# Performance work log

Measured on AMD Instinct MI355X. Metric: run time of the kernel, lower is better.

Reference implementation:

```python
import jax, jax.numpy as jnp
import numpy as np

B, L, T = 8192, 1024, 4  # batch, seq_len, n_tags (BMES)


def setup_inputs() -> dict:
    key = jax.random.key(0)
    k1, k2, k3, k4, k5 = jax.random.split(key, 5)
    return {
        "s_tag": jax.random.normal(k1, (B, L, T), dtype=jnp.float32),
        "tags": jax.random.randint(k2, (B, L), 0, T),
        "mask": jnp.ones((B, L), dtype=bool),
        "trans_score": (jax.random.normal(k3, (T, T), dtype=jnp.float32) * 0.1),
        "start_score": (jax.random.normal(k4, (T,), dtype=jnp.float32) * 0.1),
        "end_score": (jax.random.normal(k5, (T,), dtype=jnp.float32) * 0.1),
    }


def reference(s_tag, tags, mask, trans_score, start_score, end_score):
    # forward() path of LinearCRFWordSegmentation: loss = (logZ - gold_score)/B.
    # Note: forward calls set_mask(False), so the structural masks are unused.
    b, l, t = s_tag.shape
    bidx = jnp.arange(b)
    end_pos = mask.sum(axis=-1) - 1  # [B] index of last valid position

    # ---- gold path score (get_scores) ----
    emit = jnp.take_along_axis(s_tag, tags[..., None], axis=-1)[..., 0]  # [B,L]
    trans = trans_score[tags[:, :-1], tags[:, 1:]]                        # [B,L-1]
    per_pos = emit + jnp.pad(trans, ((0, 0), (1, 0)))                     # [B,L]
    score = jnp.sum(jnp.where(mask, per_pos, jnp.float32(0)))
    score = score + start_score[tags[:, 0]].sum()
    score = score + end_score[tags[bidx, end_pos]].sum()

    # ---- log partition (crf): sequential logsumexp recurrence over tags ----
    s0 = s_tag[:, 0] + start_score  # [B,T]

    def step(s_prev, emit_t):
        # [B,T_prev,1] + [1,T_prev,T_cur] + [B,1,T_cur] -> logsumexp over prev
        s_new = jax.nn.logsumexp(
            s_prev[:, :, None] + trans_score[None] + emit_t[:, None, :], axis=1
        )
        return s_new, s_new

    emits = jnp.swapaxes(s_tag, 0, 1)  # [L,B,T]
    _, ss = jax.lax.scan(step, s0, emits[1:])      # [L-1,B,T]
    ss = jnp.concatenate([s0[None], ss], axis=0)    # [L,B,T] alpha trellis
    final = ss[end_pos, bidx] + end_score           # [B,T]
    logZ = jax.nn.logsumexp(final, axis=-1).sum()

    return (logZ - score) / jnp.float32(b)
```

## Files before the change

### kernel.cpp

```cpp
#include <hip/hip_runtime.h>

#define Bn 8192
#define Ln 1024

#define LOG2E 1.4426950408889634f
#define LN2f  0.6931471805599453f

typedef float f32x2 __attribute__((ext_vector_type(2)));
typedef __attribute__((address_space(3))) void lds_void_t;
typedef const __attribute__((address_space(1))) void gbl_void_t;

__device__ __forceinline__ float sel4(float4 v, int t) {
    float r = v.x;
    r = (t == 1) ? v.y : r;
    r = (t == 2) ? v.z : r;
    r = (t == 3) ? v.w : r;
    return r;
}

__device__ __forceinline__ float rfl(float x) {
    return __int_as_float(__builtin_amdgcn_readfirstlane(__float_as_int(x)));
}

__device__ __forceinline__ f32x2 pkmax(f32x2 a, f32x2 b) {
    return (f32x2){fmaxf(a.x, b.x), fmaxf(a.y, b.y)};
}

__global__ __launch_bounds__(64) void crf_half(
    const float* __restrict__ s_tag, const int* __restrict__ tags,
    const float* __restrict__ trans,
    float* __restrict__ wsP, int* __restrict__ wsK, float* __restrict__ wsS)
{
    __shared__ float4 sS[512];

    const int lw = threadIdx.x;
    const int b  = blockIdx.x >> 1;
    const int h  = blockIdx.x & 1;

    const float4* __restrict__ srow = (const float4*)s_tag + (size_t)b * Ln + h * 512;
    const int*    __restrict__ trow = tags + (size_t)b * Ln + h * 512;

#pragma unroll
    for (int k = 0; k < 8; k++) {
        int s = k * 64 + lw;
        int g = s ^ ((s >> 3) & 7);
        __builtin_amdgcn_global_load_lds((gbl_void_t*)(srow + g),
                                         (lds_void_t*)(&sS[k * 64]), 16, 0, 0);
    }

    const int4* trow4 = (const int4*)(trow + 8 * lw);
    int4 ta = trow4[0], tb = trow4[1];
    int tg[8] = {ta.x, ta.y, ta.z, ta.w, tb.x, tb.y, tb.z, tb.w};
    int prevtag = 0;
    if (!(h == 0 && lw == 0)) prevtag = trow[8 * lw - 1];

    float trsum = 0.f;
    {
        int pt = prevtag;
#pragma unroll
        for (int j = 0; j < 8; j++) {
            if (!(h == 0 && lw == 0 && j == 0)) trsum += trans[pt * 4 + tg[j]];
            pt = tg[j];
        }
    }
    float es[4][4];
#pragma unroll
    for (int k = 0; k < 4; k++)
#pragma unroll
        for (int j = 0; j < 4; j++)
            es[k][j] = rfl(exp2f(trans[k * 4 + j] * LOG2E));

    asm volatile("s_waitcnt vmcnt(0)" ::: "memory");

    float4 st[8];
#pragma unroll
    for (int j = 0; j < 8; j++)
        st[j] = sS[8 * lw + (j ^ (lw & 7))];

    f32x2 pc[4][2];
#pragma unroll
    for (int j = 0; j < 4; j++) {
        pc[j][0] = (f32x2){(j == 0) ? 1.f : 0.f, (j == 1) ? 1.f : 0.f};
        pc[j][1] = (f32x2){(j == 2) ? 1.f : 0.f, (j == 3) ? 1.f : 0.f};
    }
    int scale = 0;
    float emitsum = 0.f;

#pragma unroll
    for (int j = 0; j < 8; j++) {
        emitsum += sel4(st[j], tg[j]);
        if (!(j == 0 && lw == 0 && h == 0)) {
            float f0 = exp2f(st[j].x * LOG2E);
            float f1 = exp2f(st[j].y * LOG2E);
            float f2 = exp2f(st[j].z * LOG2E);
            float f3 = exp2f(st[j].w * LOG2E);

            f32x2 n00 = pc[0][0] * es[0][0] + pc[1][0] * es[1][0] + pc[2][0] * es[2][0] + pc[3][0] * es[3][0];
            f32x2 n01 = pc[0][1] * es[0][0] + pc[1][1] * es[1][0] + pc[2][1] * es[2][0] + pc[3][1] * es[3][0];
            f32x2 n10 = pc[0][0] * es[0][1] + pc[1][0] * es[1][1] + pc[2][0] * es[2][1] + pc[3][0] * es[3][1];
            f32x2 n11 = pc[0][1] * es[0][1] + pc[1][1] * es[1][1] + pc[2][1] * es[2][1] + pc[3][1] * es[3][1];
            f32x2 n20 = pc[0][0] * es[0][2] + pc[1][0] * es[1][2] + pc[2][0] * es[2][2] + pc[3][0] * es[3][2];
            f32x2 n21 = pc[0][1] * es[0][2] + pc[1][1] * es[1][2] + pc[2][1] * es[2][2] + pc[3][1] * es[3][2];
            f32x2 n30 = pc[0][0] * es[0][3] + pc[1][0] * es[1][3] + pc[2][0] * es[2][3] + pc[3][0] * es[3][3];
            f32x2 n31 = pc[0][1] * es[0][3] + pc[1][1] * es[1][3] + pc[2][1] * es[2][3] + pc[3][1] * es[3][3];
            pc[0][0] = n00 * f0; pc[0][1] = n01 * f0;
            pc[1][0] = n10 * f1; pc[1][1] = n11 * f1;
            pc[2][0] = n20 * f2; pc[2][1] = n21 * f2;
            pc[3][0] = n30 * f3; pc[3][1] = n31 * f3;
        }
    }
    {
        f32x2 mm = pkmax(pkmax(pkmax(pc[0][0], pc[0][1]), pkmax(pc[1][0], pc[1][1])),
                         pkmax(pkmax(pc[2][0], pc[2][1]), pkmax(pc[3][0], pc[3][1])));
        float mx = fmaxf(mm.x, mm.y);
        unsigned eb = (__float_as_uint(mx) >> 23) & 0xffu;
        scale += (int)eb - 126;
        float ms = __uint_as_float((unsigned)(253 - eb) << 23);
#pragma unroll
        for (int jj = 0; jj < 4; jj++) { pc[jj][0] *= ms; pc[jj][1] *= ms; }
    }

    float sc = emitsum + trsum;
#pragma unroll
    for (int m = 1; m < 64; m <<= 1) sc += __shfl_xor(sc, m);
    if (lw == 0) wsS[(size_t)b * 2 + h] = sc;

    float p[4][4];
#pragma unroll
    for (int i = 0; i < 4; i++)
#pragma unroll
        for (int j = 0; j < 4; j++) p[i][j] = pc[j][i >> 1][i & 1];

#pragma unroll
    for (int s = 0; s < 3; s++) {
        const int m = 1 << s;
        float q[4][4];
#pragma unroll
        for (int i = 0; i < 4; i++)
#pragma unroll
            for (int j = 0; j < 4; j++) q[i][j] = __shfl_xor(p[i][j], m);
        int sc2 = __shfl_xor(scale, m);
        bool upper = (lw & m) != 0;
        float A[4][4], Bm[4][4];
#pragma unroll
        for (int i = 0; i < 4; i++)
#pragma unroll
            for (int j = 0; j < 4; j++) {
                A[i][j]  = upper ? q[i][j] : p[i][j];
                Bm[i][j] = upper ? p[i][j] : q[i][j];
            }
#pragma unroll
        for (int i = 0; i < 4; i++)
#pragma unroll
            for (int j = 0; j < 4; j++)
                p[i][j] = A[i][0] * Bm[0][j] + A[i][1] * Bm[1][j]
                        + A[i][2] * Bm[2][j] + A[i][3] * Bm[3][j];
        scale += sc2;

        float mx = p[0][0];
#pragma unroll
        for (int i = 0; i < 4; i++)
#pragma unroll
            for (int j = 0; j < 4; j++) mx = fmaxf(mx, p[i][j]);
        unsigned eb = (__float_as_uint(mx) >> 23) & 0xffu;
        scale += (int)eb - 126;
        float ms = __uint_as_float((unsigned)(253 - eb) << 23);
#pragma unroll
        for (int i = 0; i < 4; i++)
#pragma unroll
            for (int j = 0; j < 4; j++) p[i][j] *= ms;
    }

    if ((lw & 7) == 0) {
        size_t idx = (size_t)b * 16 + h * 8 + (lw >> 3);
        float4* P4 = (float4*)wsP + idx * 4;
        P4[0] = make_float4(p[0][0], p[0][1], p[0][2], p[0][3]);
        P4[1] = make_float4(p[1][0], p[1][1], p[1][2], p[1][3]);
        P4[2] = make_float4(p[2][0], p[2][1], p[2][2], p[2][3]);
        P4[3] = make_float4(p[3][0], p[3][1], p[3][2], p[3][3]);
        wsK[idx] = scale;
    }
}

__global__ __launch_bounds__(256) void crf_fin(
    const float* __restrict__ s_tag, const int* __restrict__ tags,
    const float* __restrict__ start_s, const float* __restrict__ end_s,
    const float* __restrict__ wsP, const int* __restrict__ wsK,
    const float* __restrict__ wsS, float* __restrict__ diffs)
{
    const int t = threadIdx.x;
    const int sub = t & 15;
    const int b = blockIdx.x * 16 + (t >> 4);

    const float4* P4 = (const float4*)wsP + ((size_t)b * 16 + sub) * 4;
    float4 r0 = P4[0], r1 = P4[1], r2 = P4[2], r3 = P4[3];
    float p[4][4] = {{r0.x, r0.y, r0.z, r0.w}, {r1.x, r1.y, r1.z, r1.w},
                     {r2.x, r2.y, r2.z, r2.w}, {r3.x, r3.y, r3.z, r3.w}};
    int scale = wsK[(size_t)b * 16 + sub];

#pragma unroll
    for (int s = 0; s < 4; s++) {
        const int m = 1 << s;
        float q[4][4];
#pragma unroll
        for (int i = 0; i < 4; i++)
#pragma unroll
            for (int j = 0; j < 4; j++) q[i][j] = __shfl_xor(p[i][j], m);
        int sc2 = __shfl_xor(scale, m);
        bool upper = (sub & m) != 0;
        float A[4][4], Bm[4][4];
#pragma unroll
        for (int i = 0; i < 4; i++)
#pragma unroll
            for (int j = 0; j < 4; j++) {
                A[i][j]  = upper ? q[i][j] : p[i][j];
                Bm[i][j] = upper ? p[i][j] : q[i][j];
            }
#pragma unroll
        for (int i = 0; i < 4; i++)
#pragma unroll
            for (int j = 0; j < 4; j++)
                p[i][j] = A[i][0] * Bm[0][j] + A[i][1] * Bm[1][j]
                        + A[i][2] * Bm[2][j] + A[i][3] * Bm[3][j];
        scale += sc2;

        float mx = p[0][0];
#pragma unroll
        for (int i = 0; i < 4; i++)
#pragma unroll
            for (int j = 0; j < 4; j++) mx = fmaxf(mx, p[i][j]);
        unsigned eb = (__float_as_uint(mx) >> 23) & 0xffu;
        scale += (int)eb - 126;
        float ms = __uint_as_float((unsigned)(253 - eb) << 23);
#pragma unroll
        for (int i = 0; i < 4; i++)
#pragma unroll
            for (int j = 0; j < 4; j++) p[i][j] *= ms;
    }

    if (sub == 0) {
        float4 st0 = *((const float4*)s_tag + (size_t)b * Ln);
        float a0 = exp2f((st0.x + start_s[0]) * LOG2E);
        float a1 = exp2f((st0.y + start_s[1]) * LOG2E);
        float a2 = exp2f((st0.z + start_s[2]) * LOG2E);
        float a3 = exp2f((st0.w + start_s[3]) * LOG2E);

        float n0 = a0 * p[0][0] + a1 * p[1][0] + a2 * p[2][0] + a3 * p[3][0];
        float n1 = a0 * p[0][1] + a1 * p[1][1] + a2 * p[2][1] + a3 * p[3][1];
        float n2 = a0 * p[0][2] + a1 * p[1][2] + a2 * p[2][2] + a3 * p[3][2];
        float n3 = a0 * p[0][3] + a1 * p[1][3] + a2 * p[2][3] + a3 * p[3][3];

        float sfin = n0 * exp2f(end_s[0] * LOG2E) + n1 * exp2f(end_s[1] * LOG2E)
                   + n2 * exp2f(end_s[2] * LOG2E) + n3 * exp2f(end_s[3] * LOG2E);
        float logZ = (log2f(sfin) + (float)scale) * LN2f;

        int t0 = tags[(size_t)b * Ln];
        int tE = tags[(size_t)b * Ln + Ln - 1];
        float gold = wsS[(size_t)b * 2] + wsS[(size_t)b * 2 + 1]
                   + start_s[t0] + end_s[tE];
        diffs[b] = logZ - gold;
    }
}

__global__ __launch_bounds__(1024) void crf_pass3(
    const float* __restrict__ diffs, float* __restrict__ out)
{
    __shared__ float sm[1024];
    float s = 0.f;
    for (int i = threadIdx.x; i < Bn; i += 1024) s += diffs[i];
    sm[threadIdx.x] = s;
    __syncthreads();
    for (int off = 512; off > 0; off >>= 1) {
        if ((int)threadIdx.x < off) sm[threadIdx.x] += sm[threadIdx.x + off];
        __syncthreads();
    }
    if (threadIdx.x == 0) out[0] = sm[0] / (float)Bn;
}

extern "C" void kernel_launch(void* const* d_in, const int* in_sizes, int n_in,
                              void* d_out, int out_size, void* d_ws, size_t ws_size,
                              hipStream_t stream)
{
    const float* s_tag  = (const float*)d_in[0];
    const int*   tags   = (const int*)d_in[1];
    const float* trans  = (const float*)d_in[3];
    const float* starts = (const float*)d_in[4];
    const float* ends   = (const float*)d_in[5];

    float* wsP  = (float*)d_ws;
    int*   wsK  = (int*)(wsP + (size_t)Bn * 16 * 16);
    float* wsS  = (float*)(wsK + (size_t)Bn * 16);
    float* diffs = wsS + (size_t)Bn * 2;

    crf_half<<<dim3(Bn * 2), dim3(64), 0, stream>>>(
        s_tag, tags, trans, wsP, wsK, wsS);
    crf_fin<<<dim3(Bn / 16), dim3(256), 0, stream>>>(
        s_tag, tags, starts, ends, wsP, wsK, wsS, diffs);
    crf_pass3<<<dim3(1), dim3(1024), 0, stream>>>(diffs, (float*)d_out);
}
```

Before: 53.14 us.

## Process whole sequence per wave with double-buffered half loads

Each 64-lane block now handles a full batch row instead of a half, so there are half as many blocks. The second half's global-to-LDS loads are issued up front and waited on with a partial vmcnt, so they overlap with computing the first half. Transition-score gathers now use lane shuffles from a register instead of global loads, previous tags come from shuffles rather than extra loads, and the gold score is reduced once per row. The cost is more LDS and registers per block and less parallelism across blocks, which could lower occupancy or latency hiding.

```diff
diff --git a/kernel.cpp b/kernel.cpp
--- a/kernel.cpp
+++ b/kernel.cpp
@@ -26,70 +26,22 @@
     return (f32x2){fmaxf(a.x, b.x), fmaxf(a.y, b.y)};
 }
 
-__global__ __launch_bounds__(64) void crf_half(
-    const float* __restrict__ s_tag, const int* __restrict__ tags,
-    const float* __restrict__ trans,
-    float* __restrict__ wsP, int* __restrict__ wsK, float* __restrict__ wsS)
-{
-    __shared__ float4 sS[512];
-
-    const int lw = threadIdx.x;
-    const int b  = blockIdx.x >> 1;
-    const int h  = blockIdx.x & 1;
-
-    const float4* __restrict__ srow = (const float4*)s_tag + (size_t)b * Ln + h * 512;
-    const int*    __restrict__ trow = tags + (size_t)b * Ln + h * 512;
-
-#pragma unroll
-    for (int k = 0; k < 8; k++) {
-        int s = k * 64 + lw;
-        int g = s ^ ((s >> 3) & 7);
-        __builtin_amdgcn_global_load_lds((gbl_void_t*)(srow + g),
-                                         (lds_void_t*)(&sS[k * 64]), 16, 0, 0);
-    }
-
-    const int4* trow4 = (const int4*)(trow + 8 * lw);
-    int4 ta = trow4[0], tb = trow4[1];
-    int tg[8] = {ta.x, ta.y, ta.z, ta.w, tb.x, tb.y, tb.z, tb.w};
-    int prevtag = 0;
-    if (!(h == 0 && lw == 0)) prevtag = trow[8 * lw - 1];
-
-    float trsum = 0.f;
-    {
-        int pt = prevtag;
-#pragma unroll
-        for (int j = 0; j < 8; j++) {
-            if (!(h == 0 && lw == 0 && j == 0)) trsum += trans[pt * 4 + tg[j]];
-            pt = tg[j];
-        }
-    }
-    float es[4][4];
-#pragma unroll
-    for (int k = 0; k < 4; k++)
-#pragma unroll
-        for (int j = 0; j < 4; j++)
-            es[k][j] = rfl(exp2f(trans[k * 4 + j] * LOG2E));
-
-    asm volatile("s_waitcnt vmcnt(0)" ::: "memory");
-
-    float4 st[8];
-#pragma unroll
-    for (int j = 0; j < 8; j++)
-        st[j] = sS[8 * lw + (j ^ (lw & 7))];
-
+template <bool FIRST>
+__device__ __forceinline__ void tile8(
+    const float4 st[8], const int tg[8], const float es[4][4],
+    float p[4][4], int& scale, float& emitsum)
+{
     f32x2 pc[4][2];
 #pragma unroll
     for (int j = 0; j < 4; j++) {
         pc[j][0] = (f32x2){(j == 0) ? 1.f : 0.f, (j == 1) ? 1.f : 0.f};
         pc[j][1] = (f32x2){(j == 2) ? 1.f : 0.f, (j == 3) ? 1.f : 0.f};
     }
-    int scale = 0;
-    float emitsum = 0.f;
 
 #pragma unroll
     for (int j = 0; j < 8; j++) {
         emitsum += sel4(st[j], tg[j]);
-        if (!(j == 0 && lw == 0 && h == 0)) {
+        if (!(FIRST && j == 0)) {
             float f0 = exp2f(st[j].x * LOG2E);
             float f1 = exp2f(st[j].y * LOG2E);
             float f2 = exp2f(st[j].z * LOG2E);
@@ -119,18 +71,13 @@
 #pragma unroll
         for (int jj = 0; jj < 4; jj++) { pc[jj][0] *= ms; pc[jj][1] *= ms; }
     }
-
-    float sc = emitsum + trsum;
-#pragma unroll
-    for (int m = 1; m < 64; m <<= 1) sc += __shfl_xor(sc, m);
-    if (lw == 0) wsS[(size_t)b * 2 + h] = sc;
-
-    float p[4][4];
 #pragma unroll
     for (int i = 0; i < 4; i++)
 #pragma unroll
         for (int j = 0; j < 4; j++) p[i][j] = pc[j][i >> 1][i & 1];
-
+}
+
+__device__ __forceinline__ void butterfly3(float p[4][4], int& scale, int lw) {
 #pragma unroll
     for (int s = 0; s < 3; s++) {
         const int m = 1 << s;
@@ -170,15 +117,123 @@
 #pragma unroll
             for (int j = 0; j < 4; j++) p[i][j] *= ms;
     }
+}
+
+__global__ __launch_bounds__(64) void crf_batch(
+    const float* __restrict__ s_tag, const int* __restrict__ tags,
+    const float* __restrict__ trans,
+    float* __restrict__ wsP, int* __restrict__ wsK, float* __restrict__ wsS)
+{
+    __shared__ float4 sA[512];
+    __shared__ float4 sB[512];
+
+    const int lw = threadIdx.x;
+    const int b  = blockIdx.x;
+
+    const float4* __restrict__ srow = (const float4*)s_tag + (size_t)b * Ln;
+    const int*    __restrict__ trow = tags + (size_t)b * Ln;
+
+    float vtr = trans[lw & 15];
+
+#pragma unroll
+    for (int k = 0; k < 8; k++) {
+        int s = k * 64 + lw;
+        int g = s ^ ((s >> 3) & 7);
+        __builtin_amdgcn_global_load_lds((gbl_void_t*)(srow + g),
+                                         (lds_void_t*)(&sA[k * 64]), 16, 0, 0);
+    }
+
+    const int4* trow4 = (const int4*)trow;
+    int4 a0 = trow4[2 * lw], a1 = trow4[2 * lw + 1];
+    int4 b0 = trow4[128 + 2 * lw], b1 = trow4[129 + 2 * lw];
+
+#pragma unroll
+    for (int k = 0; k < 8; k++) {
+        int s = k * 64 + lw;
+        int g = s ^ ((s >> 3) & 7);
+        __builtin_amdgcn_global_load_lds((gbl_void_t*)(srow + 512 + g),
+                                         (lds_void_t*)(&sB[k * 64]), 16, 0, 0);
+    }
+
+    int tgA[8] = {a0.x, a0.y, a0.z, a0.w, a1.x, a1.y, a1.z, a1.w};
+    int tgB[8] = {b0.x, b0.y, b0.z, b0.w, b1.x, b1.y, b1.z, b1.w};
+
+    int prevA = __shfl(tgA[7], (lw + 63) & 63);
+    int upB   = __shfl(tgB[7], (lw + 63) & 63);
+    int a63   = __shfl(tgA[7], 63);
+    int prevB = (lw == 0) ? a63 : upB;
+
+    float trsum = 0.f;
+    {
+        int pt = prevA;
+#pragma unroll
+        for (int j = 0; j < 8; j++) {
+            float g = __shfl(vtr, pt * 4 + tgA[j]);
+            if (!(lw == 0 && j == 0)) trsum += g;
+            pt = tgA[j];
+        }
+        pt = prevB;
+#pragma unroll
+        for (int j = 0; j < 8; j++) {
+            trsum += __shfl(vtr, pt * 4 + tgB[j]);
+            pt = tgB[j];
+        }
+    }
+
+    float es[4][4];
+#pragma unroll
+    for (int k = 0; k < 4; k++)
+#pragma unroll
+        for (int j = 0; j < 4; j++)
+            es[k][j] = rfl(exp2f(trans[k * 4 + j] * LOG2E));
+
+    asm volatile("s_waitcnt vmcnt(8)" ::: "memory");
+
+    float4 stA[8];
+#pragma unroll
+    for (int j = 0; j < 8; j++)
+        stA[j] = sA[8 * lw + (j ^ (lw & 7))];
+
+    float pA[4][4];
+    int scaleA = 0;
+    float emitsum = 0.f;
+    if (lw == 0) tile8<true >(stA, tgA, es, pA, scaleA, emitsum);
+    else         tile8<false>(stA, tgA, es, pA, scaleA, emitsum);
+    butterfly3(pA, scaleA, lw);
+
+    asm volatile("s_waitcnt vmcnt(0)" ::: "memory");
+
+    float4 stB[8];
+#pragma unroll
+    for (int j = 0; j < 8; j++)
+        stB[j] = sB[8 * lw + (j ^ (lw & 7))];
+
+    float pB[4][4];
+    int scaleB = 0;
+    tile8<false>(stB, tgB, es, pB, scaleB, emitsum);
+    butterfly3(pB, scaleB, lw);
+
+    float sc = emitsum + trsum;
+#pragma unroll
+    for (int m = 1; m < 64; m <<= 1) sc += __shfl_xor(sc, m);
+    if (lw == 0) wsS[b] = sc;
 
     if ((lw & 7) == 0) {
-        size_t idx = (size_t)b * 16 + h * 8 + (lw >> 3);
-        float4* P4 = (float4*)wsP + idx * 4;
-        P4[0] = make_float4(p[0][0], p[0][1], p[0][2], p[0][3]);
-        P4[1] = make_float4(p[1][0], p[1][1], p[1][2], p[1][3]);
-        P4[2] = make_float4(p[2][0], p[2][1], p[2][2], p[2][3]);
-        P4[3] = make_float4(p[3][0], p[3][1], p[3][2], p[3][3]);
-        wsK[idx] = scale;
+        int gidx = lw >> 3;
+        size_t iA = (size_t)b * 16 + gidx;
+        size_t iB = iA + 8;
+        float4* PA = (float4*)wsP + iA * 4;
+        PA[0] = make_float4(pA[0][0], pA[0][1], pA[0][2], pA[0][3]);
+        PA[1] = make_float4(pA[1][0], pA[1][1], pA[1][2], pA[1][3]);
+        PA[2] = make_float4(pA[2][0], pA[2][1], pA[2][2], pA[2][3]);
+        PA[3] = make_float4(pA[3][0], pA[3][1], pA[3][2], pA[3][3]);
+        float4* PB = (float4*)wsP + iB * 4;
+        PB[0] = make_float4(pB[0][0], pB[0][1], pB[0][2], pB[0][3]);
+        PB[1] = make_float4(pB[1][0], pB[1][1], pB[1][2], pB[1][3]);
+        PB[2] = make_float4(pB[2][0], pB[2][1], pB[2][2], pB[2][3]);
+        PB[3] = make_float4(pB[3][0], pB[3][1], pB[3][2], pB[3][3]);
+        wsK[iA] = scaleA;
+        wsK[iB] = scaleB;
     }
 }
 
@@ -256,8 +311,7 @@
 
         int t0 = tags[(size_t)b * Ln];
         int tE = tags[(size_t)b * Ln + Ln - 1];
-        float gold = wsS[(size_t)b * 2] + wsS[(size_t)b * 2 + 1]
-                   + start_s[t0] + end_s[tE];
+        float gold = wsS[b] + start_s[t0] + end_s[tE];
         diffs[b] = logZ - gold;
     }
 }
@@ -287,12 +341,12 @@
     const float* starts = (const float*)d_in[4];
     const float* ends   = (const float*)d_in[5];
 
-    float* wsP  = (float*)d_ws;
-    int*   wsK  = (int*)(wsP + (size_t)Bn * 16 * 16);
-    float* wsS  = (float*)(wsK + (size_t)Bn * 16);
-    float* diffs = wsS + (size_t)Bn * 2;
-
-    crf_half<<<dim3(Bn * 2), dim3(64), 0, stream>>>(
+    float* wsP   = (float*)d_ws;
+    int*   wsK   = (int*)(wsP + (size_t)Bn * 16 * 16);
+    float* wsS   = (float*)(wsK + (size_t)Bn * 16);
+    float* diffs = wsS + Bn;
+
+    crf_batch<<<dim3(Bn), dim3(64), 0, stream>>>(
         s_tag, tags, trans, wsP, wsK, wsS);
     crf_fin<<<dim3(Bn / 16), dim3(256), 0, stream>>>(
         s_tag, tags, starts, ends, wsP, wsK, wsS, diffs);
```

After: 65.33 us. +22.9%, slower.

## Make half-row kernel persistent with double-buffered LDS prefetch of next chunk

Applied to the files above, without the earlier changes.

Replaces the one-block-per-half-row launch with 2560 persistent 64-thread blocks that each walk 6-7 consecutive half-rows. The next half-row's emissions are prefetched into a second LDS buffer, and its tags into registers, while the current one is computed, so load latency overlaps the matrix chain. It also swaps exp2f for the raw v_exp_f32 instruction, looks up transitions with a shuffle instead of a global gather, and carries the previous tag across chunks. The risks are fixed vmcnt wait counts that must match the number of outstanding loads, and less parallelism per block.

```diff
diff --git a/kernel.cpp b/kernel.cpp
--- a/kernel.cpp
+++ b/kernel.cpp
@@ -2,6 +2,8 @@
 
 #define Bn 8192
 #define Ln 1024
+#define NBLK 2560
+#define NHALF (Bn * 2)
 
 #define LOG2E 1.4426950408889634f
 #define LN2f  0.6931471805599453f
@@ -22,78 +24,35 @@
     return __int_as_float(__builtin_amdgcn_readfirstlane(__float_as_int(x)));
 }
 
+__device__ __forceinline__ float fexp2(float x) {
+    float r;
+    asm("v_exp_f32 %0, %1" : "=v"(r) : "v"(x));
+    return r;
+}
+
 __device__ __forceinline__ f32x2 pkmax(f32x2 a, f32x2 b) {
     return (f32x2){fmaxf(a.x, b.x), fmaxf(a.y, b.y)};
 }
 
-__global__ __launch_bounds__(64) void crf_half(
-    const float* __restrict__ s_tag, const int* __restrict__ tags,
-    const float* __restrict__ trans,
-    float* __restrict__ wsP, int* __restrict__ wsK, float* __restrict__ wsS)
-{
-    __shared__ float4 sS[512];
-
-    const int lw = threadIdx.x;
-    const int b  = blockIdx.x >> 1;
-    const int h  = blockIdx.x & 1;
-
-    const float4* __restrict__ srow = (const float4*)s_tag + (size_t)b * Ln + h * 512;
-    const int*    __restrict__ trow = tags + (size_t)b * Ln + h * 512;
-
-#pragma unroll
-    for (int k = 0; k < 8; k++) {
-        int s = k * 64 + lw;
-        int g = s ^ ((s >> 3) & 7);
-        __builtin_amdgcn_global_load_lds((gbl_void_t*)(srow + g),
-                                         (lds_void_t*)(&sS[k * 64]), 16, 0, 0);
-    }
-
-    const int4* trow4 = (const int4*)(trow + 8 * lw);
-    int4 ta = trow4[0], tb = trow4[1];
-    int tg[8] = {ta.x, ta.y, ta.z, ta.w, tb.x, tb.y, tb.z, tb.w};
-    int prevtag = 0;
-    if (!(h == 0 && lw == 0)) prevtag = trow[8 * lw - 1];
-
-    float trsum = 0.f;
-    {
-        int pt = prevtag;
-#pragma unroll
-        for (int j = 0; j < 8; j++) {
-            if (!(h == 0 && lw == 0 && j == 0)) trsum += trans[pt * 4 + tg[j]];
-            pt = tg[j];
-        }
-    }
-    float es[4][4];
-#pragma unroll
-    for (int k = 0; k < 4; k++)
-#pragma unroll
-        for (int j = 0; j < 4; j++)
-            es[k][j] = rfl(exp2f(trans[k * 4 + j] * LOG2E));
-
-    asm volatile("s_waitcnt vmcnt(0)" ::: "memory");
-
-    float4 st[8];
-#pragma unroll
-    for (int j = 0; j < 8; j++)
-        st[j] = sS[8 * lw + (j ^ (lw & 7))];
-
+__device__ __forceinline__ void tile8(
+    const float4 st[8], const int tg[8], const float es[4][4],
+    float p[4][4], int& scale, float& emitsum, bool skip0)
+{
     f32x2 pc[4][2];
 #pragma unroll
     for (int j = 0; j < 4; j++) {
         pc[j][0] = (f32x2){(j == 0) ? 1.f : 0.f, (j == 1) ? 1.f : 0.f};
         pc[j][1] = (f32x2){(j == 2) ? 1.f : 0.f, (j == 3) ? 1.f : 0.f};
     }
-    int scale = 0;
-    float emitsum = 0.f;
 
 #pragma unroll
     for (int j = 0; j < 8; j++) {
         emitsum += sel4(st[j], tg[j]);
-        if (!(j == 0 && lw == 0 && h == 0)) {
-            float f0 = exp2f(st[j].x * LOG2E);
-            float f1 = exp2f(st[j].y * LOG2E);
-            float f2 = exp2f(st[j].z * LOG2E);
-            float f3 = exp2f(st[j].w * LOG2E);
+        if (!(skip0 && j == 0)) {
+            float f0 = fexp2(st[j].x * LOG2E);
+            float f1 = fexp2(st[j].y * LOG2E);
+            float f2 = fexp2(st[j].z * LOG2E);
+            float f3 = fexp2(st[j].w * LOG2E);
 
             f32x2 n00 = pc[0][0] * es[0][0] + pc[1][0] * es[1][0] + pc[2][0] * es[2][0] + pc[3][0] * es[3][0];
             f32x2 n01 = pc[0][1] * es[0][0] + pc[1][1] * es[1][0] + pc[2][1] * es[2][0] + pc[3][1] * es[3][0];
@@ -119,18 +78,13 @@
 #pragma unroll
         for (int jj = 0; jj < 4; jj++) { pc[jj][0] *= ms; pc[jj][1] *= ms; }
     }
-
-    float sc = emitsum + trsum;
-#pragma unroll
-    for (int m = 1; m < 64; m <<= 1) sc += __shfl_xor(sc, m);
-    if (lw == 0) wsS[(size_t)b * 2 + h] = sc;
-
-    float p[4][4];
 #pragma unroll
     for (int i = 0; i < 4; i++)
 #pragma unroll
         for (int j = 0; j < 4; j++) p[i][j] = pc[j][i >> 1][i & 1];
-
+}
+
+__device__ __forceinline__ void butterfly3(float p[4][4], int& scale, int lw) {
 #pragma unroll
     for (int s = 0; s < 3; s++) {
         const int m = 1 << s;
@@ -170,15 +124,125 @@
 #pragma unroll
             for (int j = 0; j < 4; j++) p[i][j] *= ms;
     }
-
-    if ((lw & 7) == 0) {
-        size_t idx = (size_t)b * 16 + h * 8 + (lw >> 3);
-        float4* P4 = (float4*)wsP + idx * 4;
-        P4[0] = make_float4(p[0][0], p[0][1], p[0][2], p[0][3]);
-        P4[1] = make_float4(p[1][0], p[1][1], p[1][2], p[1][3]);
-        P4[2] = make_float4(p[2][0], p[2][1], p[2][2], p[2][3]);
-        P4[3] = make_float4(p[3][0], p[3][1], p[3][2], p[3][3]);
-        wsK[idx] = scale;
+}
+
+__global__ __launch_bounds__(64) void crf_pers(
+    const float* __restrict__ s_tag, const int* __restrict__ tags,
+    const float* __restrict__ trans,
+    float* __restrict__ wsP, int* __restrict__ wsK, float* __restrict__ wsS)
+{
+    __shared__ float4 sS[1024];
+
+    const int lw  = threadIdx.x;
+    const int bid = blockIdx.x;
+    const int start = bid * 6 + (bid < 1024 ? bid : 1024);
+    const int n     = 6 + (bid < 1024 ? 1 : 0);
+
+    const float4* __restrict__ s4 = (const float4*)s_tag;
+
+    float vtr = trans[lw & 15];
+    int pidx = start * 512 - 1; if (pidx < 0) pidx = 0;
+    int carry0 = tags[pidx];
+
+    float es[4][4];
+#pragma unroll
+    for (int k = 0; k < 4; k++)
+#pragma unroll
+        for (int j = 0; j < 4; j++)
+            es[k][j] = rfl(fexp2(trans[k * 4 + j] * LOG2E));
+
+    asm volatile("s_waitcnt vmcnt(0) lgkmcnt(0)" ::: "memory");
+    int prev_carry = carry0;
+
+    {
+        const float4* src = s4 + (size_t)start * 512;
+#pragma unroll
+        for (int k = 0; k < 8; k++) {
+            int s = k * 64 + lw;
+            int g = s ^ ((s >> 3) & 7);
+            __builtin_amdgcn_global_load_lds((gbl_void_t*)(src + g),
+                                             (lds_void_t*)(&sS[k * 64]), 16, 0, 0);
+        }
+    }
+    const int4* tr4 = (const int4*)tags;
+    int4 ca = tr4[(size_t)start * 128 + 2 * lw];
+    int4 cb = tr4[(size_t)start * 128 + 2 * lw + 1];
+
+    for (int i = 0; i < n; i++) {
+        const int hi = start + i;
+        const bool has_next = (i + 1 < n);
+
+        int4 na, nb;
+        if (has_next) {
+            const float4* src = s4 + (size_t)(hi + 1) * 512;
+            float4* dst = &sS[((i + 1) & 1) * 512];
+#pragma unroll
+            for (int k = 0; k < 8; k++) {
+                int s = k * 64 + lw;
+                int g = s ^ ((s >> 3) & 7);
+                __builtin_amdgcn_global_load_lds((gbl_void_t*)(src + g),
+                                                 (lds_void_t*)(dst + k * 64), 16, 0, 0);
+            }
+            na = tr4[(size_t)(hi + 1) * 128 + 2 * lw];
+            nb = tr4[(size_t)(hi + 1) * 128 + 2 * lw + 1];
+        }
+
+        if (i == 0) {
+            if (has_next) asm volatile("s_waitcnt vmcnt(10)" ::: "memory");
+            else          asm volatile("s_waitcnt vmcnt(0)"  ::: "memory");
+        } else if (has_next) {
+            asm volatile("s_waitcnt vmcnt(16)" ::: "memory");
+        } else {
+            asm volatile("s_waitcnt vmcnt(6)"  ::: "memory");
+        }
+
+        const float4* buf = &sS[(i & 1) * 512];
+        int tg[8] = {ca.x, ca.y, ca.z, ca.w, cb.x, cb.y, cb.z, cb.w};
+
+        float4 st[8];
+#pragma unroll
+        for (int j = 0; j < 8; j++)
+            st[j] = buf[8 * lw + (j ^ (lw & 7))];
+
+        const bool skip0 = (hi == 0) && (lw == 0);
+
+        int pl = __shfl(tg[7], (lw + 63) & 63);
+        int prev = (lw == 0) ? prev_carry : pl;
+
+        float trsum = 0.f;
+        {
+            int pt = prev;
+#pragma unroll
+            for (int j = 0; j < 8; j++) {
+                float g = __shfl(vtr, pt * 4 + tg[j]);
+                trsum += (skip0 && j == 0) ? 0.f : g;
+                pt = tg[j];
+            }
+        }
+
+        float p[4][4];
+        int scale = 0;
+        float emitsum = 0.f;
+        tile8(st, tg, es, p, scale, emitsum, skip0);
+        butterfly3(p, scale, lw);
+
+        float sc = emitsum + trsum;
+#pragma unroll
+        for (int m = 1; m < 64; m <<= 1) sc += __shfl_xor(sc, m);
+
+        if ((lw & 7) == 0) {
+            size_t idx = (size_t)hi * 8 + (lw >> 3);
+            float4* P4 = (float4*)wsP + idx * 4;
+            P4[0] = make_float4(p[0][0], p[0][1], p[0][2], p[0][3]);
+            P4[1] = make_float4(p[1][0], p[1][1], p[1][2], p[1][3]);
+            P4[2] = make_float4(p[2][0], p[2][1], p[2][2], p[2][3]);
+            P4[3] = make_float4(p[3][0], p[3][1], p[3][2], p[3][3]);
+            wsK[idx] = scale;
+        }
+        if (lw == 0) wsS[hi] = sc;
+
+        prev_carry = __shfl(tg[7], 63);
+        ca = na; cb = nb;
     }
 }
 
@@ -287,12 +351,12 @@
     const float* starts = (const float*)d_in[4];
     const float* ends   = (const float*)d_in[5];
 
-    float* wsP  = (float*)d_ws;
-    int*   wsK  = (int*)(wsP + (size_t)Bn * 16 * 16);
-    float* wsS  = (float*)(wsK + (size_t)Bn * 16);
+    float* wsP   = (float*)d_ws;
+    int*   wsK   = (int*)(wsP + (size_t)Bn * 16 * 16);
+    float* wsS   = (float*)(wsK + (size_t)Bn * 16);
     float* diffs = wsS + (size_t)Bn * 2;
 
-    crf_half<<<dim3(Bn * 2), dim3(64), 0, stream>>>(
+    crf_pers<<<dim3(NBLK), dim3(64), 0, stream>>>(
         s_tag, tags, trans, wsP, wsK, wsS);
     crf_fin<<<dim3(Bn / 16), dim3(256), 0, stream>>>(
         s_tag, tags, starts, ends, wsP, wsK, wsS, diffs);
```

Result: slower. 58.75 us (+10.6%).

## Replace async LDS loads with register loads and shuffle-based transition gather

Applied to the files above, without the earlier changes.

Replaces the global_load_lds async copy with coalesced register loads that are then written to LDS, and fetches the previous tag via a cross-lane shuffle instead of a separate global load. Transition-score lookups for the gold path now come from a wave-wide shuffle of a register holding the 4x4 matrix rather than indexed global reads. exp2f is replaced by a raw v_exp_f32 inline asm, and the body is split into helper functions. It trades the async-copy path for explicit register staging, which may change latency hiding, while cutting scattered small global reads.

```diff
diff --git a/kernel.cpp b/kernel.cpp
--- a/kernel.cpp
+++ b/kernel.cpp
@@ -7,8 +7,6 @@
 #define LN2f  0.6931471805599453f
 
 typedef float f32x2 __attribute__((ext_vector_type(2)));
-typedef __attribute__((address_space(3))) void lds_void_t;
-typedef const __attribute__((address_space(1))) void gbl_void_t;
 
 __device__ __forceinline__ float sel4(float4 v, int t) {
     float r = v.x;
@@ -22,78 +20,35 @@
     return __int_as_float(__builtin_amdgcn_readfirstlane(__float_as_int(x)));
 }
 
+__device__ __forceinline__ float fexp2(float x) {
+    float r;
+    asm("v_exp_f32 %0, %1" : "=v"(r) : "v"(x));
+    return r;
+}
+
 __device__ __forceinline__ f32x2 pkmax(f32x2 a, f32x2 b) {
     return (f32x2){fmaxf(a.x, b.x), fmaxf(a.y, b.y)};
 }
 
-__global__ __launch_bounds__(64) void crf_half(
-    const float* __restrict__ s_tag, const int* __restrict__ tags,
-    const float* __restrict__ trans,
-    float* __restrict__ wsP, int* __restrict__ wsK, float* __restrict__ wsS)
-{
-    __shared__ float4 sS[512];
-
-    const int lw = threadIdx.x;
-    const int b  = blockIdx.x >> 1;
-    const int h  = blockIdx.x & 1;
-
-    const float4* __restrict__ srow = (const float4*)s_tag + (size_t)b * Ln + h * 512;
-    const int*    __restrict__ trow = tags + (size_t)b * Ln + h * 512;
-
-#pragma unroll
-    for (int k = 0; k < 8; k++) {
-        int s = k * 64 + lw;
-        int g = s ^ ((s >> 3) & 7);
-        __builtin_amdgcn_global_load_lds((gbl_void_t*)(srow + g),
-                                         (lds_void_t*)(&sS[k * 64]), 16, 0, 0);
-    }
-
-    const int4* trow4 = (const int4*)(trow + 8 * lw);
-    int4 ta = trow4[0], tb = trow4[1];
-    int tg[8] = {ta.x, ta.y, ta.z, ta.w, tb.x, tb.y, tb.z, tb.w};
-    int prevtag = 0;
-    if (!(h == 0 && lw == 0)) prevtag = trow[8 * lw - 1];
-
-    float trsum = 0.f;
-    {
-        int pt = prevtag;
-#pragma unroll
-        for (int j = 0; j < 8; j++) {
-            if (!(h == 0 && lw == 0 && j == 0)) trsum += trans[pt * 4 + tg[j]];
-            pt = tg[j];
-        }
-    }
-    float es[4][4];
-#pragma unroll
-    for (int k = 0; k < 4; k++)
-#pragma unroll
-        for (int j = 0; j < 4; j++)
-            es[k][j] = rfl(exp2f(trans[k * 4 + j] * LOG2E));
-
-    asm volatile("s_waitcnt vmcnt(0)" ::: "memory");
-
-    float4 st[8];
-#pragma unroll
-    for (int j = 0; j < 8; j++)
-        st[j] = sS[8 * lw + (j ^ (lw & 7))];
-
+__device__ __forceinline__ void tile8(
+    const float4 st[8], const int tg[8], const float es[4][4],
+    float p[4][4], int& scale, float& emitsum, bool skip0)
+{
     f32x2 pc[4][2];
 #pragma unroll
     for (int j = 0; j < 4; j++) {
         pc[j][0] = (f32x2){(j == 0) ? 1.f : 0.f, (j == 1) ? 1.f : 0.f};
         pc[j][1] = (f32x2){(j == 2) ? 1.f : 0.f, (j == 3) ? 1.f : 0.f};
     }
-    int scale = 0;
-    float emitsum = 0.f;
 
 #pragma unroll
     for (int j = 0; j < 8; j++) {
         emitsum += sel4(st[j], tg[j]);
-        if (!(j == 0 && lw == 0 && h == 0)) {
-            float f0 = exp2f(st[j].x * LOG2E);
-            float f1 = exp2f(st[j].y * LOG2E);
-            float f2 = exp2f(st[j].z * LOG2E);
-            float f3 = exp2f(st[j].w * LOG2E);
+        if (!(skip0 && j == 0)) {
+            float f0 = fexp2(st[j].x * LOG2E);
+            float f1 = fexp2(st[j].y * LOG2E);
+            float f2 = fexp2(st[j].z * LOG2E);
+            float f3 = fexp2(st[j].w * LOG2E);
 
             f32x2 n00 = pc[0][0] * es[0][0] + pc[1][0] * es[1][0] + pc[2][0] * es[2][0] + pc[3][0] * es[3][0];
             f32x2 n01 = pc[0][1] * es[0][0] + pc[1][1] * es[1][0] + pc[2][1] * es[2][0] + pc[3][1] * es[3][0];
@@ -119,18 +74,13 @@
 #pragma unroll
         for (int jj = 0; jj < 4; jj++) { pc[jj][0] *= ms; pc[jj][1] *= ms; }
     }
-
-    float sc = emitsum + trsum;
-#pragma unroll
-    for (int m = 1; m < 64; m <<= 1) sc += __shfl_xor(sc, m);
-    if (lw == 0) wsS[(size_t)b * 2 + h] = sc;
-
-    float p[4][4];
 #pragma unroll
     for (int i = 0; i < 4; i++)
 #pragma unroll
         for (int j = 0; j < 4; j++) p[i][j] = pc[j][i >> 1][i & 1];
-
+}
+
+__device__ __forceinline__ void butterfly3(float p[4][4], int& scale, int lw) {
 #pragma unroll
     for (int s = 0; s < 3; s++) {
         const int m = 1 << s;
@@ -170,9 +120,76 @@
 #pragma unroll
             for (int j = 0; j < 4; j++) p[i][j] *= ms;
     }
+}
+
+__global__ __launch_bounds__(64) void crf_half(
+    const float* __restrict__ s_tag, const int* __restrict__ tags,
+    const float* __restrict__ trans,
+    float* __restrict__ wsP, int* __restrict__ wsK, float* __restrict__ wsS)
+{
+    __shared__ float4 sS[512];
+
+    const int lw = threadIdx.x;
+    const int hb = blockIdx.x;
+
+    const float4* __restrict__ srow = (const float4*)s_tag + (size_t)hb * 512;
+    const int*    __restrict__ trow = tags + (size_t)hb * 512;
+
+    int prev_c = trow[(hb == 0) ? 0 : -1];
+
+    const int4* trow4 = (const int4*)trow;
+    int4 ta = trow4[2 * lw], tb = trow4[2 * lw + 1];
+
+    const int swl = lw ^ ((lw >> 3) & 7);
+    float4 v[8];
+#pragma unroll
+    for (int k = 0; k < 8; k++) v[k] = srow[64 * k + swl];
+
+    int tg[8] = {ta.x, ta.y, ta.z, ta.w, tb.x, tb.y, tb.z, tb.w};
+    const bool skip0 = (hb == 0) && (lw == 0);
+
+    int pl = __shfl(tg[7], (lw + 63) & 63);
+    int prev = (lw == 0) ? prev_c : pl;
+
+    float vtr = trans[lw & 15];
+    float trsum = 0.f;
+    {
+        int pt = prev;
+#pragma unroll
+        for (int j = 0; j < 8; j++) {
+            float g = __shfl(vtr, pt * 4 + tg[j]);
+            trsum += (skip0 && j == 0) ? 0.f : g;
+            pt = tg[j];
+        }
+    }
+    float es[4][4];
+#pragma unroll
+    for (int k = 0; k < 4; k++)
+#pragma unroll
+        for (int j = 0; j < 4; j++)
+            es[k][j] = rfl(fexp2(trans[k * 4 + j] * LOG2E));
+
+#pragma unroll
+    for (int k = 0; k < 8; k++) sS[64 * k + lw] = v[k];
+
+    float4 st[8];
+#pragma unroll
+    for (int j = 0; j < 8; j++)
+        st[j] = sS[8 * lw + (j ^ (lw & 7))];
+
+    float p[4][4];
+    int scale = 0;
+    float emitsum = 0.f;
+    tile8(st, tg, es, p, scale, emitsum, skip0);
+    butterfly3(p, scale, lw);
+
+    float sc = emitsum + trsum;
+#pragma unroll
+    for (int m = 1; m < 64; m <<= 1) sc += __shfl_xor(sc, m);
+    if (lw == 0) wsS[hb] = sc;
 
     if ((lw & 7) == 0) {
-        size_t idx = (size_t)b * 16 + h * 8 + (lw >> 3);
+        size_t idx = (size_t)hb * 8 + (lw >> 3);
         float4* P4 = (float4*)wsP + idx * 4;
         P4[0] = make_float4(p[0][0], p[0][1], p[0][2], p[0][3]);
         P4[1] = make_float4(p[1][0], p[1][1], p[1][2], p[1][3]);
@@ -287,9 +304,9 @@
     const float* starts = (const float*)d_in[4];
     const float* ends   = (const float*)d_in[5];
 
-    float* wsP  = (float*)d_ws;
-    int*   wsK  = (int*)(wsP + (size_t)Bn * 16 * 16);
-    float* wsS  = (float*)(wsK + (size_t)Bn * 16);
+    float* wsP   = (float*)d_ws;
+    int*   wsK   = (int*)(wsP + (size_t)Bn * 16 * 16);
+    float* wsS   = (float*)(wsK + (size_t)Bn * 16);
     float* diffs = wsS + (size_t)Bn * 2;
 
     crf_half<<<dim3(Bn * 2), dim3(64), 0, stream>>>(
```

Result: faster. 50.03 us (-5.8%).
